# Optimization experiments

Measured on AMD Instinct MI355X. Metric: run time of the kernel, lower is better.

## Reference

```python
import jax, jax.numpy as jnp
import numpy as np

B, T, D = 512, 256, 256
U = 512  # lstm_units


def setup_inputs() -> dict:
    key = jax.random.key(0)
    ks = jax.random.split(key, 8)
    s_in = 1.0 / np.sqrt(D)
    s_h = 1.0 / np.sqrt(U)
    return {
        "x": jax.random.normal(ks[0], (B, T, D), dtype=jnp.float32),
        "Wx": jax.random.normal(ks[1], (D, 4 * U), dtype=jnp.float32) * s_in,
        "Wh": jax.random.normal(ks[2], (U, 4 * U), dtype=jnp.float32) * s_h,
        "b": jax.random.normal(ks[3], (4 * U,), dtype=jnp.float32) * 0.01,
        "W1": jax.random.normal(ks[4], (U, 128), dtype=jnp.float32) * s_h,
        "b1": jnp.zeros((128,), dtype=jnp.float32),
        "W2": jax.random.normal(ks[5], (128, 10), dtype=jnp.float32) * (1.0 / np.sqrt(128)),
        "b2": jnp.zeros((10,), dtype=jnp.float32),
    }


def _lstm_last_hidden(x, Wx, Wh, b):
    # Precompute input projections for all timesteps: [B,T,4U] -> scan axis T
    xz = jnp.einsum("btd,dg->tbg", x, Wx) + b  # [T,B,4U]

    def step(carry, xz_t):
        h, c = carry
        z = xz_t + h @ Wh  # [B,4U]
        i, f, g, o = jnp.split(z, 4, axis=-1)  # keras gate order: i,f,c,o
        i = jax.nn.sigmoid(i)
        f = jax.nn.sigmoid(f)
        g = jnp.tanh(g)
        o = jax.nn.sigmoid(o)
        c = f * c + i * g
        h = o * jnp.tanh(c)
        return (h, c), None

    h0 = jnp.zeros((x.shape[0], Wh.shape[0]), dtype=x.dtype)
    (h, _), _ = jax.lax.scan(step, (h0, h0), xz)
    return h  # last hidden state [B,U]


def reference(x, Wx, Wh, b, W1, b1, W2, b2):
    h = _lstm_last_hidden(x, Wx, Wh, b)
    h = jax.nn.relu(h @ W1 + b1)
    return jax.nn.softmax(h @ W2 + b2, axis=-1)
```

## Files before the change

kernel.cpp:

```cpp
#include <hip/hip_runtime.h>

#define B_SZ 512
#define T_SZ 256
#define D_SZ 256
#define U_SZ 512

typedef float  f32x4  __attribute__((ext_vector_type(4)));
typedef short  short8 __attribute__((ext_vector_type(8)));
typedef __bf16 bf16x8 __attribute__((ext_vector_type(8)));

static __device__ __forceinline__ unsigned short f2bf(float f) {
  unsigned u = __builtin_bit_cast(unsigned, f);
  return (unsigned short)((u + 0x7FFFu + ((u >> 16) & 1u)) >> 16);
}

static __device__ __forceinline__ f32x4 mfma_bf16(short8 a, short8 b, f32x4 c) {
  return __builtin_amdgcn_mfma_f32_16x16x32_bf16(
      __builtin_bit_cast(bf16x8, a), __builtin_bit_cast(bf16x8, b), c, 0, 0, 0);
}

static __device__ __forceinline__ float sigm(float x) {
  return 1.f / (1.f + __expf(-x));
}
static __device__ __forceinline__ float tanh_fast(float x) {
  return 1.f - 2.f / (__expf(2.f * x) + 1.f);
}

__global__ __launch_bounds__(256) void wt_kernel(const float* __restrict__ Wx,
                                                 const float* __restrict__ Wh,
                                                 unsigned short* __restrict__ Wt) {
  __shared__ float tile[32][33];
  const int ct = blockIdx.x;
  const int kt = blockIdx.y;
  const int tx = threadIdx.x & 31;
  const int ty = threadIdx.x >> 5;
  const int k0 = kt * 32;
#pragma unroll
  for (int q = 0; q < 4; ++q) {
    int kl = ty + q * 8;
    int kg = k0 + kl;
    float v = (kg < 256) ? Wx[(size_t)kg * 2048 + ct * 32 + tx]
                         : Wh[(size_t)(kg - 256) * 2048 + ct * 32 + tx];
    tile[kl][tx] = v;
  }
  __syncthreads();
#pragma unroll
  for (int q = 0; q < 4; ++q) {
    int cl = ty + q * 8;
    Wt[(size_t)(ct * 32 + cl) * 768 + k0 + tx] = f2bf(tile[tx][cl]);
  }
}

__global__ __launch_bounds__(256, 1) void lstm_kernel(
    const float* __restrict__ x, const unsigned short* __restrict__ Wt,
    const float* __restrict__ bias, unsigned short* __restrict__ hbuf,
    unsigned* __restrict__ flags, float* __restrict__ hfin) {
  extern __shared__ char smem[];
  const int tid  = threadIdx.x;
  const int lane = tid & 63;
  const int wv   = tid >> 6;
  const int mt   = wv & 1;
  const int uh   = wv >> 1;
  const int g    = blockIdx.x & 15;
  const int s    = blockIdx.x >> 4;
  const int col  = lane & 15;
  const int kgrp = lane >> 4;
  const int ug   = s * 32 + uh * 16 + col;

  short8 Bfr[96];
#pragma unroll
  for (int kt = 0; kt < 24; ++kt) {
#pragma unroll
    for (int gg = 0; gg < 4; ++gg) {
      const unsigned short* p =
          Wt + (size_t)(gg * 512 + ug) * 768 + kgrp * 8 + kt * 32;
      Bfr[kt * 4 + gg] = *(const short8*)p;
    }
  }
  float bias_g[4];
#pragma unroll
  for (int gg = 0; gg < 4; ++gg) bias_g[gg] = bias[gg * 512 + ug];

#pragma unroll
  for (int i = 0; i < 4; ++i) {
    int ch = tid + i * 256;
    int row = ch >> 5;
    int k0 = (ch & 31) * 8;
    const float* xp = x + ((size_t)(g * 32 + row) * T_SZ + 0) * D_SZ + k0;
    float4 a  = *(const float4*)xp;
    float4 b2 = *(const float4*)(xp + 4);
    short8 v;
    v[0] = (short)f2bf(a.x);  v[1] = (short)f2bf(a.y);
    v[2] = (short)f2bf(a.z);  v[3] = (short)f2bf(a.w);
    v[4] = (short)f2bf(b2.x); v[5] = (short)f2bf(b2.y);
    v[6] = (short)f2bf(b2.z); v[7] = (short)f2bf(b2.w);
    unsigned byte = ((unsigned)(row * 512 + k0 * 2)) ^ ((row & 7) << 4);
    *(short8*)(smem + byte) = v;
  }

  f32x4 cst = {0.f, 0.f, 0.f, 0.f};
  int p = 0;
  int par = 0;
  for (int t = 0; t < 256; ++t) {
    float4 xa[4], xb[4];
    if (t < 255) {
#pragma unroll
      for (int i = 0; i < 4; ++i) {
        int ch = tid + i * 256;
        int row = ch >> 5;
        int k0 = (ch & 31) * 8;
        const float* xp =
            x + ((size_t)(g * 32 + row) * T_SZ + (t + 1)) * D_SZ + k0;
        xa[i] = *(const float4*)xp;
        xb[i] = *(const float4*)(xp + 4);
      }
    }

    if (t > 0) {
      const unsigned* fb = flags + (((unsigned)(g << 8) + (t - 1)) << 4);
      if (lane < 16) {
        while (__hip_atomic_load(fb + lane, __ATOMIC_RELAXED,
                                 __HIP_MEMORY_SCOPE_AGENT) == 0u) {
        }
      }
      __builtin_amdgcn_sched_barrier(0);
    }

    const unsigned short* hr =
        hbuf + ((size_t)p << 18) + ((size_t)(g * 32) << 9);
#pragma unroll
    for (int i = 0; i < 16; ++i) {
      int ch = tid + i * 256;
      int row = ch >> 7;
      int c4 = ch & 127;
      const unsigned long long* hp =
          (const unsigned long long*)(hr + ((size_t)row << 9) + c4 * 4);
      unsigned long long v = __hip_atomic_load(hp, __ATOMIC_RELAXED,
                                               __HIP_MEMORY_SCOPE_AGENT);
      unsigned byte =
          (32768u + (unsigned)(row * 1024 + c4 * 8)) ^ ((row & 7) << 4);
      *(unsigned long long*)(smem + byte) = v;
    }
    __syncthreads();

    if (t < 255) {
#pragma unroll
      for (int i = 0; i < 4; ++i) {
        int ch = tid + i * 256;
        int row = ch >> 5;
        int k0 = (ch & 31) * 8;
        short8 v;
        v[0] = (short)f2bf(xa[i].x);  v[1] = (short)f2bf(xa[i].y);
        v[2] = (short)f2bf(xa[i].z);  v[3] = (short)f2bf(xa[i].w);
        v[4] = (short)f2bf(xb[i].x);  v[5] = (short)f2bf(xb[i].y);
        v[6] = (short)f2bf(xb[i].z);  v[7] = (short)f2bf(xb[i].w);
        unsigned byte = ((unsigned)((par ^ 1) * 16384 + row * 512 + k0 * 2)) ^
                        ((row & 7) << 4);
        *(short8*)(smem + byte) = v;
      }
    }

    f32x4 acc[4];
#pragma unroll
    for (int gg = 0; gg < 4; ++gg) acc[gg] = (f32x4){0.f, 0.f, 0.f, 0.f};
    const int arow = mt * 16 + col;
    const unsigned rsw = (unsigned)((arow & 7) << 4);
#pragma unroll
    for (int kt = 0; kt < 24; ++kt) {
      unsigned byte;
      if (kt < 8)
        byte = ((unsigned)(par * 16384 + arow * 512 + kt * 64 + kgrp * 16)) ^ rsw;
      else
        byte = (32768u +
                (unsigned)(arow * 1024 + (kt - 8) * 64 + kgrp * 16)) ^ rsw;
      short8 af = *(const short8*)(smem + byte);
      acc[0] = mfma_bf16(af, Bfr[kt * 4 + 0], acc[0]);
      acc[1] = mfma_bf16(af, Bfr[kt * 4 + 1], acc[1]);
      acc[2] = mfma_bf16(af, Bfr[kt * 4 + 2], acc[2]);
      acc[3] = mfma_bf16(af, Bfr[kt * 4 + 3], acc[3]);
    }

#pragma unroll
    for (int j = 0; j < 4; ++j) {
      float zi = acc[0][j] + bias_g[0];
      float zf = acc[1][j] + bias_g[1];
      float zg = acc[2][j] + bias_g[2];
      float zo = acc[3][j] + bias_g[3];
      float ii = sigm(zi);
      float ff = sigm(zf);
      float gv = tanh_fast(zg);
      float oo = sigm(zo);
      float cv = ff * cst[j] + ii * gv;
      cst[j] = cv;
      float hv = oo * tanh_fast(cv);
      int brow = g * 32 + mt * 16 + kgrp * 4 + j;
      if (t == 255) {
        hfin[(size_t)brow * 512 + ug] = hv;
      } else {
        unsigned short* hp =
            hbuf + (((size_t)(p ^ 1)) << 18) + ((size_t)brow << 9) + ug;
        __hip_atomic_store(hp, f2bf(hv), __ATOMIC_RELAXED,
                           __HIP_MEMORY_SCOPE_AGENT);
      }
    }

    if (t == 255) break;

    __syncthreads();
    if (tid == 0) {
      __hip_atomic_store(flags + ((((unsigned)(g << 8) + t) << 4) + s), 1u,
                         __ATOMIC_RELAXED, __HIP_MEMORY_SCOPE_AGENT);
    }
    p ^= 1;
    par ^= 1;
  }
}

__global__ __launch_bounds__(128) void mlp_kernel(
    const float* __restrict__ hfin, const float* __restrict__ W1,
    const float* __restrict__ b1, const float* __restrict__ W2,
    const float* __restrict__ b2, float* __restrict__ out) {
  __shared__ float hrow[512];
  __shared__ float act[128];
  __shared__ float lg[10];
  const int b = blockIdx.x;
  const int tid = threadIdx.x;
#pragma unroll
  for (int i = 0; i < 4; ++i)
    hrow[tid + i * 128] = hfin[(size_t)b * 512 + tid + i * 128];
  __syncthreads();
  float s = b1[tid];
#pragma unroll 8
  for (int k = 0; k < 512; ++k) s += hrow[k] * W1[(size_t)k * 128 + tid];
  act[tid] = fmaxf(s, 0.f);
  __syncthreads();
  if (tid < 10) {
    float l = b2[tid];
#pragma unroll 8
    for (int k = 0; k < 128; ++k) l += act[k] * W2[(size_t)k * 10 + tid];
    lg[tid] = l;
  }
  __syncthreads();
  if (tid == 0) {
    float m = lg[0];
    for (int j = 1; j < 10; ++j) m = fmaxf(m, lg[j]);
    float e[10];
    float sum = 0.f;
    for (int j = 0; j < 10; ++j) {
      e[j] = expf(lg[j] - m);
      sum += e[j];
    }
    float inv = 1.f / sum;
    for (int j = 0; j < 10; ++j) out[(size_t)b * 10 + j] = e[j] * inv;
  }
}

extern "C" void kernel_launch(void* const* d_in, const int* in_sizes, int n_in,
                              void* d_out, int out_size, void* d_ws,
                              size_t ws_size, hipStream_t stream) {
  const float* x    = (const float*)d_in[0];
  const float* Wx   = (const float*)d_in[1];
  const float* Wh   = (const float*)d_in[2];
  const float* bias = (const float*)d_in[3];
  const float* W1   = (const float*)d_in[4];
  const float* b1   = (const float*)d_in[5];
  const float* W2   = (const float*)d_in[6];
  const float* b2   = (const float*)d_in[7];
  float* out = (float*)d_out;

  char* ws = (char*)d_ws;
  unsigned short* hbuf = (unsigned short*)ws;
  unsigned* flags      = (unsigned*)(ws + 1048576);
  unsigned short* Wt   = (unsigned short*)(ws + 2097152);
  float* hfin          = (float*)(ws + 2097152 + 3145728);

  hipMemsetAsync(d_ws, 0, 1048576 + 262144, stream);

  wt_kernel<<<dim3(64, 24), 256, 0, stream>>>(Wx, Wh, Wt);

  hipFuncSetAttribute((const void*)lstm_kernel,
                      hipFuncAttributeMaxDynamicSharedMemorySize, 65536);
  lstm_kernel<<<256, 256, 65536, stream>>>(x, Wt, bias, hbuf, flags, hfin);

  mlp_kernel<<<512, 128, 0, stream>>>(hfin, W1, b1, W2, b2, out);
}
```

Before: 2.832 ms.

## Pipeline four batch chunks per block to hide cross-block sync latency

```diff
diff --git a/kernel.cpp b/kernel.cpp
--- a/kernel.cpp
+++ b/kernel.cpp
@@ -59,13 +59,11 @@
   const int tid  = threadIdx.x;
   const int lane = tid & 63;
   const int wv   = tid >> 6;
-  const int mt   = wv & 1;
-  const int uh   = wv >> 1;
-  const int g    = blockIdx.x & 15;
-  const int s    = blockIdx.x >> 4;
+  const int P    = blockIdx.x & 7;
+  const int s    = blockIdx.x >> 3;
   const int col  = lane & 15;
   const int kgrp = lane >> 4;
-  const int ug   = s * 32 + uh * 16 + col;
+  const int ug   = s * 64 + wv * 16 + col;
 
   short8 Bfr[96];
 #pragma unroll
@@ -81,138 +79,115 @@
 #pragma unroll
   for (int gg = 0; gg < 4; ++gg) bias_g[gg] = bias[gg * 512 + ug];
 
-#pragma unroll
-  for (int i = 0; i < 4; ++i) {
-    int ch = tid + i * 256;
-    int row = ch >> 5;
-    int k0 = (ch & 31) * 8;
-    const float* xp = x + ((size_t)(g * 32 + row) * T_SZ + 0) * D_SZ + k0;
-    float4 a  = *(const float4*)xp;
-    float4 b2 = *(const float4*)(xp + 4);
-    short8 v;
-    v[0] = (short)f2bf(a.x);  v[1] = (short)f2bf(a.y);
-    v[2] = (short)f2bf(a.z);  v[3] = (short)f2bf(a.w);
-    v[4] = (short)f2bf(b2.x); v[5] = (short)f2bf(b2.y);
-    v[6] = (short)f2bf(b2.z); v[7] = (short)f2bf(b2.w);
-    unsigned byte = ((unsigned)(row * 512 + k0 * 2)) ^ ((row & 7) << 4);
-    *(short8*)(smem + byte) = v;
-  }
-
-  f32x4 cst = {0.f, 0.f, 0.f, 0.f};
+  f32x4 cst[4];
+#pragma unroll
+  for (int c = 0; c < 4; ++c) cst[c] = (f32x4){0.f, 0.f, 0.f, 0.f};
+
   int p = 0;
-  int par = 0;
   for (int t = 0; t < 256; ++t) {
-    float4 xa[4], xb[4];
-    if (t < 255) {
-#pragma unroll
-      for (int i = 0; i < 4; ++i) {
+#pragma unroll
+    for (int c = 0; c < 4; ++c) {
+      const int RG = P * 4 + c;
+      const unsigned cbase = (unsigned)c * 24576u;
+
+      if (t > 0) {
+        const unsigned* fb = flags + ((((unsigned)RG << 8) + (t - 1)) << 3);
+        if (lane < 8) {
+          while (__hip_atomic_load(fb + lane, __ATOMIC_RELAXED,
+                                   __HIP_MEMORY_SCOPE_AGENT) == 0u) {
+          }
+        }
+        __builtin_amdgcn_sched_barrier(0);
+      }
+
+#pragma unroll
+      for (int i = 0; i < 2; ++i) {
         int ch = tid + i * 256;
         int row = ch >> 5;
         int k0 = (ch & 31) * 8;
         const float* xp =
-            x + ((size_t)(g * 32 + row) * T_SZ + (t + 1)) * D_SZ + k0;
-        xa[i] = *(const float4*)xp;
-        xb[i] = *(const float4*)(xp + 4);
-      }
-    }
-
-    if (t > 0) {
-      const unsigned* fb = flags + (((unsigned)(g << 8) + (t - 1)) << 4);
-      if (lane < 16) {
-        while (__hip_atomic_load(fb + lane, __ATOMIC_RELAXED,
-                                 __HIP_MEMORY_SCOPE_AGENT) == 0u) {
+            x + ((size_t)(RG * 16 + row) * T_SZ + t) * D_SZ + k0;
+        float4 a  = *(const float4*)xp;
+        float4 b2 = *(const float4*)(xp + 4);
+        short8 v;
+        v[0] = (short)f2bf(a.x);  v[1] = (short)f2bf(a.y);
+        v[2] = (short)f2bf(a.z);  v[3] = (short)f2bf(a.w);
+        v[4] = (short)f2bf(b2.x); v[5] = (short)f2bf(b2.y);
+        v[6] = (short)f2bf(b2.z); v[7] = (short)f2bf(b2.w);
+        unsigned byte =
+            (cbase + (unsigned)(row * 512 + k0 * 2)) ^ ((row & 7) << 4);
+        *(short8*)(smem + byte) = v;
+      }
+      const unsigned short* hr =
+          hbuf + ((size_t)p << 18) + ((size_t)(RG * 16) << 9);
+#pragma unroll
+      for (int i = 0; i < 8; ++i) {
+        int ch = tid + i * 256;
+        int row = ch >> 7;
+        int c4 = ch & 127;
+        const unsigned long long* hp =
+            (const unsigned long long*)(hr + ((size_t)row << 9) + c4 * 4);
+        unsigned long long v = __hip_atomic_load(hp, __ATOMIC_RELAXED,
+                                                 __HIP_MEMORY_SCOPE_AGENT);
+        unsigned byte = (cbase + 8192u + (unsigned)(row * 1024 + c4 * 8)) ^
+                        ((row & 7) << 4);
+        *(unsigned long long*)(smem + byte) = v;
+      }
+      __syncthreads();
+
+      f32x4 acc[4];
+#pragma unroll
+      for (int gg = 0; gg < 4; ++gg) acc[gg] = (f32x4){0.f, 0.f, 0.f, 0.f};
+      const int arow = col;
+      const unsigned rsw = (unsigned)((arow & 7) << 4);
+#pragma unroll
+      for (int kt = 0; kt < 24; ++kt) {
+        unsigned byte;
+        if (kt < 8)
+          byte = (cbase + (unsigned)(arow * 512 + kt * 64 + kgrp * 16)) ^ rsw;
+        else
+          byte = (cbase + 8192u +
+                  (unsigned)(arow * 1024 + (kt - 8) * 64 + kgrp * 16)) ^ rsw;
+        short8 af = *(const short8*)(smem + byte);
+        acc[0] = mfma_bf16(af, Bfr[kt * 4 + 0], acc[0]);
+        acc[1] = mfma_bf16(af, Bfr[kt * 4 + 1], acc[1]);
+        acc[2] = mfma_bf16(af, Bfr[kt * 4 + 2], acc[2]);
+        acc[3] = mfma_bf16(af, Bfr[kt * 4 + 3], acc[3]);
+      }
+
+#pragma unroll
+      for (int j = 0; j < 4; ++j) {
+        float zi = acc[0][j] + bias_g[0];
+        float zf = acc[1][j] + bias_g[1];
+        float zg = acc[2][j] + bias_g[2];
+        float zo = acc[3][j] + bias_g[3];
+        float ii = sigm(zi);
+        float ff = sigm(zf);
+        float gv = tanh_fast(zg);
+        float oo = sigm(zo);
+        float cv = ff * cst[c][j] + ii * gv;
+        cst[c][j] = cv;
+        float hv = oo * tanh_fast(cv);
+        int brow = RG * 16 + kgrp * 4 + j;
+        if (t == 255) {
+          hfin[(size_t)brow * 512 + ug] = hv;
+        } else {
+          unsigned short* hp =
+              hbuf + (((size_t)(p ^ 1)) << 18) + ((size_t)brow << 9) + ug;
+          __hip_atomic_store(hp, f2bf(hv), __ATOMIC_RELAXED,
+                             __HIP_MEMORY_SCOPE_AGENT);
         }
       }
-      __builtin_amdgcn_sched_barrier(0);
-    }
-
-    const unsigned short* hr =
-        hbuf + ((size_t)p << 18) + ((size_t)(g * 32) << 9);
-#pragma unroll
-    for (int i = 0; i < 16; ++i) {
-      int ch = tid + i * 256;
-      int row = ch >> 7;
-      int c4 = ch & 127;
-      const unsigned long long* hp =
-          (const unsigned long long*)(hr + ((size_t)row << 9) + c4 * 4);
-      unsigned long long v = __hip_atomic_load(hp, __ATOMIC_RELAXED,
-                                               __HIP_MEMORY_SCOPE_AGENT);
-      unsigned byte =
-          (32768u + (unsigned)(row * 1024 + c4 * 8)) ^ ((row & 7) << 4);
-      *(unsigned long long*)(smem + byte) = v;
-    }
-    __syncthreads();
-
-    if (t < 255) {
-#pragma unroll
-      for (int i = 0; i < 4; ++i) {
-        int ch = tid + i * 256;
-        int row = ch >> 5;
-        int k0 = (ch & 31) * 8;
-        short8 v;
-        v[0] = (short)f2bf(xa[i].x);  v[1] = (short)f2bf(xa[i].y);
-        v[2] = (short)f2bf(xa[i].z);  v[3] = (short)f2bf(xa[i].w);
-        v[4] = (short)f2bf(xb[i].x);  v[5] = (short)f2bf(xb[i].y);
-        v[6] = (short)f2bf(xb[i].z);  v[7] = (short)f2bf(xb[i].w);
-        unsigned byte = ((unsigned)((par ^ 1) * 16384 + row * 512 + k0 * 2)) ^
-                        ((row & 7) << 4);
-        *(short8*)(smem + byte) = v;
-      }
-    }
-
-    f32x4 acc[4];
-#pragma unroll
-    for (int gg = 0; gg < 4; ++gg) acc[gg] = (f32x4){0.f, 0.f, 0.f, 0.f};
-    const int arow = mt * 16 + col;
-    const unsigned rsw = (unsigned)((arow & 7) << 4);
-#pragma unroll
-    for (int kt = 0; kt < 24; ++kt) {
-      unsigned byte;
-      if (kt < 8)
-        byte = ((unsigned)(par * 16384 + arow * 512 + kt * 64 + kgrp * 16)) ^ rsw;
-      else
-        byte = (32768u +
-                (unsigned)(arow * 1024 + (kt - 8) * 64 + kgrp * 16)) ^ rsw;
-      short8 af = *(const short8*)(smem + byte);
-      acc[0] = mfma_bf16(af, Bfr[kt * 4 + 0], acc[0]);
-      acc[1] = mfma_bf16(af, Bfr[kt * 4 + 1], acc[1]);
-      acc[2] = mfma_bf16(af, Bfr[kt * 4 + 2], acc[2]);
-      acc[3] = mfma_bf16(af, Bfr[kt * 4 + 3], acc[3]);
-    }
-
-#pragma unroll
-    for (int j = 0; j < 4; ++j) {
-      float zi = acc[0][j] + bias_g[0];
-      float zf = acc[1][j] + bias_g[1];
-      float zg = acc[2][j] + bias_g[2];
-      float zo = acc[3][j] + bias_g[3];
-      float ii = sigm(zi);
-      float ff = sigm(zf);
-      float gv = tanh_fast(zg);
-      float oo = sigm(zo);
-      float cv = ff * cst[j] + ii * gv;
-      cst[j] = cv;
-      float hv = oo * tanh_fast(cv);
-      int brow = g * 32 + mt * 16 + kgrp * 4 + j;
-      if (t == 255) {
-        hfin[(size_t)brow * 512 + ug] = hv;
-      } else {
-        unsigned short* hp =
-            hbuf + (((size_t)(p ^ 1)) << 18) + ((size_t)brow << 9) + ug;
-        __hip_atomic_store(hp, f2bf(hv), __ATOMIC_RELAXED,
-                           __HIP_MEMORY_SCOPE_AGENT);
-      }
-    }
-
-    if (t == 255) break;
-
-    __syncthreads();
-    if (tid == 0) {
-      __hip_atomic_store(flags + ((((unsigned)(g << 8) + t) << 4) + s), 1u,
-                         __ATOMIC_RELAXED, __HIP_MEMORY_SCOPE_AGENT);
+
+      if (t < 255) {
+        __syncthreads();
+        if (tid == 0) {
+          __hip_atomic_store(flags + ((((unsigned)RG << 8) + t) << 3) + s, 1u,
+                             __ATOMIC_RELAXED, __HIP_MEMORY_SCOPE_AGENT);
+        }
+      }
     }
     p ^= 1;
-    par ^= 1;
   }
 }
 
@@ -279,8 +254,8 @@
   wt_kernel<<<dim3(64, 24), 256, 0, stream>>>(Wx, Wh, Wt);
 
   hipFuncSetAttribute((const void*)lstm_kernel,
-                      hipFuncAttributeMaxDynamicSharedMemorySize, 65536);
-  lstm_kernel<<<256, 256, 65536, stream>>>(x, Wt, bias, hbuf, flags, hfin);
+                      hipFuncAttributeMaxDynamicSharedMemorySize, 98304);
+  lstm_kernel<<<64, 256, 98304, stream>>>(x, Wt, bias, hbuf, flags, hfin);
 
   mlp_kernel<<<512, 128, 0, stream>>>(hfin, W1, b1, W2, b2, out);
 }
```

After: 7.180 ms. 154% more time.
